# Kernel tuning notes

Measured on AMD Instinct MI355X. Metric: run time of the kernel, lower is better.

## Reference

```python
import jax, jax.numpy as jnp
import numpy as np
from jax import lax

B, T, C, H, W = 32, 64, 3, 32, 32
N_OBJS = 2
HID = 200
FEAT = N_OBJS * C * H * W  # 6*32*32 = 6144, matches LocationNetwork input


def setup_inputs() -> dict:
    key = jax.random.key(0)
    ks = jax.random.split(key, 20)

    def g(k, shape, scale):
        return jax.random.normal(k, shape, dtype=jnp.float32) * scale

    inp = {
        "x": jax.random.normal(ks[0], (B, C, H, W, T), dtype=jnp.float32),
        # shallow UNet (depth=3, base 8 channels): encoder
        "enc_w1": g(ks[1], (8, C, 3, 3), 0.2),  "enc_b1": jnp.zeros((8,), jnp.float32),
        "enc_w2": g(ks[2], (16, 8, 3, 3), 0.12), "enc_b2": jnp.zeros((16,), jnp.float32),
        "enc_w3": g(ks[3], (32, 16, 3, 3), 0.08),"enc_b3": jnp.zeros((32,), jnp.float32),
        # decoder (upsample + skip concat)
        "dec_w2": g(ks[4], (16, 48, 3, 3), 0.05), "dec_b2": jnp.zeros((16,), jnp.float32),
        "dec_w1": g(ks[5], (8, 24, 3, 3), 0.07),  "dec_b1": jnp.zeros((8,), jnp.float32),
        # final 1x1 conv -> n_objs mask logits
        "out_w": g(ks[6], (N_OBJS, 8, 1, 1), 0.3), "out_b": jnp.zeros((N_OBJS,), jnp.float32),
        # LocationNetwork: 6144 -> 200 -> 200 -> 2*n_objs
        "loc_w1": g(ks[7], (FEAT, HID), 0.013), "loc_b1": jnp.zeros((HID,), jnp.float32),
        "loc_w2": g(ks[8], (HID, HID), 0.07),   "loc_b2": jnp.zeros((HID,), jnp.float32),
        "loc_w3": g(ks[9], (HID, 2 * N_OBJS), 0.07), "loc_b3": jnp.zeros((2 * N_OBJS,), jnp.float32),
    }
    return inp


def _conv(h, w, b):
    return lax.conv_general_dilated(
        h, w, (1, 1), "SAME", dimension_numbers=("NCHW", "OIHW", "NCHW")
    ) + b[None, :, None, None]


def _pool(h):  # 2x2 max pool
    return lax.reduce_window(h, -jnp.inf, lax.max, (1, 1, 2, 2), (1, 1, 2, 2), "VALID")


def _up(h):
    return jnp.repeat(jnp.repeat(h, 2, axis=2), 2, axis=3)


def _forward(x, enc_w1, enc_b1, enc_w2, enc_b2, enc_w3, enc_b3,
             dec_w2, dec_b2, dec_w1, dec_b1, out_w, out_b,
             loc_w1, loc_b1, loc_w2, loc_b2, loc_w3, loc_b3):
    relu = jax.nn.relu
    # fold time into batch: [B,C,H,W,T] -> [B*T,C,H,W] (replaces per-t Python loop)
    xt = jnp.moveaxis(x, -1, 1).reshape(B * T, C, H, W)

    # shallow UNet, depth 3
    e1 = relu(_conv(xt, enc_w1, enc_b1))                 # [BT, 8, 32, 32]
    e2 = relu(_conv(_pool(e1), enc_w2, enc_b2))          # [BT,16, 16, 16]
    e3 = relu(_conv(_pool(e2), enc_w3, enc_b3))          # [BT,32,  8,  8]
    d2 = relu(_conv(jnp.concatenate([_up(e3), e2], 1), dec_w2, dec_b2))  # [BT,16,16,16]
    d1 = relu(_conv(jnp.concatenate([_up(d2), e1], 1), dec_w1, dec_b1))  # [BT, 8,32,32]
    logits = _conv(d1, out_w, out_b)                     # [BT, n_objs, 32, 32]

    # append ones channel, softmax over channels -> attention masks
    logits = jnp.concatenate([logits, jnp.ones_like(logits[:, :1])], axis=1)
    masks = jax.nn.softmax(logits, axis=1)               # [BT, n_objs+1, H, W]

    # masked_objs: mask_i * x, concatenated along channel dim
    masked = masks[:, :N_OBJS, None] * xt[:, None]       # [BT, n_objs, C, H, W]
    feat = masked.reshape(B * T, FEAT)                   # flatten per frame (6144)

    # LocationNetwork (batched over all B*T frames, replaces nested Python loops)
    h = jax.nn.relu(feat @ loc_w1 + loc_b1)
    h = jax.nn.relu(h @ loc_w2 + loc_b2)
    loc = h @ loc_w3 + loc_b3                            # [BT, 2*n_objs]

    loc = loc.reshape(B, T, N_OBJS, 2)
    # torch.split(h, n_objs, dim=1) + cat(dim=1) is an identity; squeeze(2) drops the
    # singleton from the per-frame reshape(-1, n_objs, 2)
    return jnp.tanh(loc) * (H / 2) + H / 2               # [B, T, n_objs, 2]


def reference(x, enc_w1, enc_b1, enc_w2, enc_b2, enc_w3, enc_b3,
              dec_w2, dec_b2, dec_w1, dec_b1, out_w, out_b,
              loc_w1, loc_b1, loc_w2, loc_b2, loc_w3, loc_b3):
    return _forward(x, enc_w1, enc_b1, enc_w2, enc_b2, enc_w3, enc_b3,
                    dec_w2, dec_b2, dec_w1, dec_b1, out_w, out_b,
                    loc_w1, loc_b1, loc_w2, loc_b2, loc_w3, loc_b3)
```

## Files before the change

kernel.cpp:

```cpp
#include <hip/hip_runtime.h>

constexpr int Bc = 32, Tc = 64, Cc = 3, Hc = 32, Wc = 32;
constexpr int F = Bc * Tc;
constexpr int FEATN = 2 * Cc * Hc * Wc;
constexpr int HID = 200;
constexpr int NP = 224;
constexpr int KSPLIT = 16;

typedef __attribute__((ext_vector_type(8))) short bf16x8;
typedef __attribute__((ext_vector_type(4))) float f32x4;

static __device__ __forceinline__ ushort f2bf(float x) {
    union { float f; unsigned u; } v; v.f = x;
    unsigned r = (v.u + 0x7FFF + ((v.u >> 16) & 1)) >> 16;
    return (ushort)r;
}

__global__ __launch_bounds__(256)
void transpose_kernel(const float* __restrict__ x, float* __restrict__ xt) {
    __shared__ float lds[32 * 65];
    int bid = blockIdx.x;
    int h = bid & 31;
    int c = (bid >> 5) % 3;
    int b = bid / (3 * 32);
    const float* src = x + (size_t)bid * 2048;
#pragma unroll
    for (int j = 0; j < 8; ++j) {
        int i = threadIdx.x + j * 256;
        lds[(i >> 6) * 65 + (i & 63)] = src[i];
    }
    __syncthreads();
#pragma unroll
    for (int j = 0; j < 8; ++j) {
        int i = threadIdx.x + j * 256;
        int t = i >> 5, w = i & 31;
        int f = b * 64 + t;
        xt[((size_t)(f * 3 + c) << 10) + h * 32 + w] = lds[w * 65 + t];
    }
}

template<int CIN1, int CIN2, int COUT, int H, int W, bool UP1, bool RELU>
__global__ __launch_bounds__(256)
void conv3x3_allco_kernel(const float* __restrict__ in1, const float* __restrict__ in2,
                          const float* __restrict__ wgt, const float* __restrict__ bias,
                          float* __restrict__ out) {
    constexpr int CTOT = CIN1 + CIN2;
    constexpr int NW = CTOT * 9 * COUT;
    constexpr int NCOG = COUT / 8;
    static_assert(COUT % 8 == 0, "COUT % 8");
    __shared__ __align__(16) float wl[NW];
    for (int i = threadIdx.x; i < NW; i += 256) {
        int co = i % COUT, r = i / COUT;
        wl[i] = wgt[co * CTOT * 9 + r];
    }
    __syncthreads();

    int tid = blockIdx.x * 256 + threadIdx.x;
    int x0  = tid % W;
    int y0  = (tid / W) % H;
    int cog = (tid / (W * H)) % NCOG;
    int f   = tid / (W * H * NCOG);

    float acc[8];
#pragma unroll
    for (int c = 0; c < 8; ++c) acc[c] = bias[cog * 8 + c];

    const float4* wl4 = reinterpret_cast<const float4*>(wl);
    const int wsel = cog * 2;

    for (int ci = 0; ci < CIN1; ++ci) {
        const float* ib;
        if (UP1) ib = in1 + (size_t)(f * CIN1 + ci) * (H / 2) * (W / 2);
        else     ib = in1 + (size_t)(f * CIN1 + ci) * H * W;
#pragma unroll
        for (int kh = 0; kh < 3; ++kh) {
            int yy = y0 + kh - 1;
            if (yy < 0 || yy >= H) continue;
#pragma unroll
            for (int kw = 0; kw < 3; ++kw) {
                int xx = x0 + kw - 1;
                if (xx < 0 || xx >= W) continue;
                float v;
                if (UP1) v = ib[(yy >> 1) * (W / 2) + (xx >> 1)];
                else     v = ib[yy * W + xx];
                int r = ci * 9 + kh * 3 + kw;
                float4 w0 = wl4[r * (COUT / 4) + wsel];
                float4 w1 = wl4[r * (COUT / 4) + wsel + 1];
                acc[0] = fmaf(v, w0.x, acc[0]); acc[1] = fmaf(v, w0.y, acc[1]);
                acc[2] = fmaf(v, w0.z, acc[2]); acc[3] = fmaf(v, w0.w, acc[3]);
                acc[4] = fmaf(v, w1.x, acc[4]); acc[5] = fmaf(v, w1.y, acc[5]);
                acc[6] = fmaf(v, w1.z, acc[6]); acc[7] = fmaf(v, w1.w, acc[7]);
            }
        }
    }
    if constexpr (CIN2 > 0) {
        for (int ci2 = 0; ci2 < CIN2; ++ci2) {
            const float* ib = in2 + (size_t)(f * CIN2 + ci2) * H * W;
#pragma unroll
            for (int kh = 0; kh < 3; ++kh) {
                int yy = y0 + kh - 1;
                if (yy < 0 || yy >= H) continue;
#pragma unroll
                for (int kw = 0; kw < 3; ++kw) {
                    int xx = x0 + kw - 1;
                    if (xx < 0 || xx >= W) continue;
                    float v = ib[yy * W + xx];
                    int r = (CIN1 + ci2) * 9 + kh * 3 + kw;
                    float4 w0 = wl4[r * (COUT / 4) + wsel];
                    float4 w1 = wl4[r * (COUT / 4) + wsel + 1];
                    acc[0] = fmaf(v, w0.x, acc[0]); acc[1] = fmaf(v, w0.y, acc[1]);
                    acc[2] = fmaf(v, w0.z, acc[2]); acc[3] = fmaf(v, w0.w, acc[3]);
                    acc[4] = fmaf(v, w1.x, acc[4]); acc[5] = fmaf(v, w1.y, acc[5]);
                    acc[6] = fmaf(v, w1.z, acc[6]); acc[7] = fmaf(v, w1.w, acc[7]);
                }
            }
        }
    }

    size_t ob = (size_t)(f * COUT + cog * 8) * (H * W) + y0 * W + x0;
#pragma unroll
    for (int c = 0; c < 8; ++c) {
        float vv = acc[c];
        if (RELU) vv = fmaxf(vv, 0.0f);
        out[ob + (size_t)c * (H * W)] = vv;
    }
}

template<int CIN1, int CIN2, int COUT, int H, int W, bool RELU>
__global__ __launch_bounds__(256)
void conv3x3_up_q22_kernel(const float* __restrict__ in1, const float* __restrict__ in2,
                           const float* __restrict__ wgt, const float* __restrict__ bias,
                           float* __restrict__ out) {
    constexpr int CTOT = CIN1 + CIN2;
    constexpr int NW = CTOT * 9 * COUT;
    constexpr int NCOG = COUT / 8;
    constexpr int H2 = H / 2, W2 = W / 2;
    static_assert(COUT % 8 == 0, "COUT % 8");
    __shared__ __align__(16) float wl[NW];
    for (int i = threadIdx.x; i < NW; i += 256) {
        int co = i % COUT, r = i / COUT;
        wl[i] = wgt[co * CTOT * 9 + r];
    }
    __syncthreads();

    int tid = blockIdx.x * 256 + threadIdx.x;
    int xq  = tid % W2;
    int yq  = (tid / W2) % H2;
    int cog = (tid / (W2 * H2)) % NCOG;
    int f   = tid / (W2 * H2 * NCOG);

    float acc[4][8];
#pragma unroll
    for (int p = 0; p < 4; ++p)
#pragma unroll
        for (int c = 0; c < 8; ++c) acc[p][c] = bias[cog * 8 + c];

    const float4* wl4 = reinterpret_cast<const float4*>(wl);
    const int wsel = cog * 2;

    const bool by0 = (yq > 0), by2 = (yq < H2 - 1);
    const bool bx0 = (xq > 0), bx2 = (xq < W2 - 1);
    const int ym = by0 ? yq - 1 : 0, yp = by2 ? yq + 1 : H2 - 1;
    const int xm = bx0 ? xq - 1 : 0, xp = bx2 ? xq + 1 : W2 - 1;

    for (int ci = 0; ci < CIN1; ++ci) {
        const float* ib = in1 + (size_t)(f * CIN1 + ci) * (H2 * W2);
        float s[3][3];
        s[0][0] = ib[ym * W2 + xm]; s[0][1] = ib[ym * W2 + xq]; s[0][2] = ib[ym * W2 + xp];
        s[1][0] = ib[yq * W2 + xm]; s[1][1] = ib[yq * W2 + xq]; s[1][2] = ib[yq * W2 + xp];
        s[2][0] = ib[yp * W2 + xm]; s[2][1] = ib[yp * W2 + xq]; s[2][2] = ib[yp * W2 + xp];
        s[0][0] = (by0 && bx0) ? s[0][0] : 0.f;
        s[0][1] = by0 ? s[0][1] : 0.f;
        s[0][2] = (by0 && bx2) ? s[0][2] : 0.f;
        s[1][0] = bx0 ? s[1][0] : 0.f;
        s[1][2] = bx2 ? s[1][2] : 0.f;
        s[2][0] = (by2 && bx0) ? s[2][0] : 0.f;
        s[2][1] = by2 ? s[2][1] : 0.f;
        s[2][2] = (by2 && bx2) ? s[2][2] : 0.f;
#pragma unroll
        for (int kh = 0; kh < 3; ++kh) {
#pragma unroll
            for (int kw = 0; kw < 3; ++kw) {
                int r = ci * 9 + kh * 3 + kw;
                float4 w0 = wl4[r * (COUT / 4) + wsel];
                float4 w1 = wl4[r * (COUT / 4) + wsel + 1];
#pragma unroll
                for (int dy = 0; dy < 2; ++dy) {
                    const int sy = (dy == 0) ? ((kh == 0) ? 0 : 1) : ((kh == 2) ? 2 : 1);
#pragma unroll
                    for (int dx = 0; dx < 2; ++dx) {
                        const int sx = (dx == 0) ? ((kw == 0) ? 0 : 1) : ((kw == 2) ? 2 : 1);
                        const float v = s[sy][sx];
                        float* a = acc[dy * 2 + dx];
                        a[0] = fmaf(v, w0.x, a[0]); a[1] = fmaf(v, w0.y, a[1]);
                        a[2] = fmaf(v, w0.z, a[2]); a[3] = fmaf(v, w0.w, a[3]);
                        a[4] = fmaf(v, w1.x, a[4]); a[5] = fmaf(v, w1.y, a[5]);
                        a[6] = fmaf(v, w1.z, a[6]); a[7] = fmaf(v, w1.w, a[7]);
                    }
                }
            }
        }
    }

    if constexpr (CIN2 > 0) {
        const int y2 = 2 * yq, x2 = 2 * xq;
        const int R0 = by0 ? y2 - 1 : 0, R3 = by2 ? y2 + 2 : H - 1;
        const int C0 = bx0 ? x2 - 1 : 0, C3 = bx2 ? x2 + 2 : W - 1;
        const int rr[4] = {R0, y2, y2 + 1, R3};
        const int cc[4] = {C0, x2, x2 + 1, C3};
        for (int ci2 = 0; ci2 < CIN2; ++ci2) {
            const float* ib = in2 + (size_t)(f * CIN2 + ci2) * (H * W);
            float t[4][4];
#pragma unroll
            for (int i = 0; i < 4; ++i)
#pragma unroll
                for (int j = 0; j < 4; ++j) t[i][j] = ib[rr[i] * W + cc[j]];
#pragma unroll
            for (int j = 0; j < 4; ++j) { t[0][j] = by0 ? t[0][j] : 0.f; t[3][j] = by2 ? t[3][j] : 0.f; }
#pragma unroll
            for (int i = 0; i < 4; ++i) { t[i][0] = bx0 ? t[i][0] : 0.f; t[i][3] = bx2 ? t[i][3] : 0.f; }
#pragma unroll
            for (int kh = 0; kh < 3; ++kh) {
#pragma unroll
                for (int kw = 0; kw < 3; ++kw) {
                    int r = (CIN1 + ci2) * 9 + kh * 3 + kw;
                    float4 w0 = wl4[r * (COUT / 4) + wsel];
                    float4 w1 = wl4[r * (COUT / 4) + wsel + 1];
#pragma unroll
                    for (int dy = 0; dy < 2; ++dy) {
#pragma unroll
                        for (int dx = 0; dx < 2; ++dx) {
                            const float v = t[dy + kh][dx + kw];
                            float* a = acc[dy * 2 + dx];
                            a[0] = fmaf(v, w0.x, a[0]); a[1] = fmaf(v, w0.y, a[1]);
                            a[2] = fmaf(v, w0.z, a[2]); a[3] = fmaf(v, w0.w, a[3]);
                            a[4] = fmaf(v, w1.x, a[4]); a[5] = fmaf(v, w1.y, a[5]);
                            a[6] = fmaf(v, w1.z, a[6]); a[7] = fmaf(v, w1.w, a[7]);
                        }
                    }
                }
            }
        }
    }

    const size_t ob = (size_t)(f * COUT + cog * 8) * (H * W);
#pragma unroll
    for (int dy = 0; dy < 2; ++dy)
#pragma unroll
        for (int dx = 0; dx < 2; ++dx) {
            const int p = dy * 2 + dx;
            const size_t pb = ob + (size_t)(2 * yq + dy) * W + (2 * xq + dx);
#pragma unroll
            for (int c = 0; c < 8; ++c) {
                float vv = acc[p][c];
                if (RELU) vv = fmaxf(vv, 0.0f);
                out[pb + (size_t)c * (H * W)] = vv;
            }
        }
}

template<int CH, int H, int W>
__global__ __launch_bounds__(256)
void pool2_kernel(const float* __restrict__ in, float* __restrict__ out) {
    int tid = blockIdx.x * 256 + threadIdx.x;
    constexpr int total = F * CH * (H / 2) * (W / 2);
    if (tid >= total) return;
    int x = tid % (W / 2);
    int y = (tid / (W / 2)) % (H / 2);
    int fc = tid / ((W / 2) * (H / 2));
    const float* ib = in + (size_t)fc * H * W + (2 * y) * W + 2 * x;
    float m = fmaxf(fmaxf(ib[0], ib[1]), fmaxf(ib[W], ib[W + 1]));
    out[tid] = m;
}

__global__ __launch_bounds__(256)
void maskfeat_kernel(const float* __restrict__ d1, const float* __restrict__ xt,
                     const float* __restrict__ ow, const float* __restrict__ ob,
                     ushort* __restrict__ feat) {
    int tid = blockIdx.x * 256 + threadIdx.x;
    if (tid >= F * 1024) return;
    int hw = tid & 1023;
    int f  = tid >> 10;
    const float* db = d1 + ((size_t)f << 13) + hw;
    float l0 = ob[0], l1 = ob[1];
#pragma unroll
    for (int c = 0; c < 8; ++c) {
        float v = db[c << 10];
        l0 = fmaf(v, ow[c], l0);
        l1 = fmaf(v, ow[8 + c], l1);
    }
    float mx = fmaxf(fmaxf(l0, l1), 1.0f);
    float e0 = expf(l0 - mx), e1 = expf(l1 - mx), e2 = expf(1.0f - mx);
    float inv = 1.0f / (e0 + e1 + e2);
    float m0 = e0 * inv, m1 = e1 * inv;
    const float* xb = xt + (size_t)f * 3072 + hw;
    ushort* fb = feat + (size_t)f * 6144 + hw;
#pragma unroll
    for (int c = 0; c < 3; ++c) {
        float xv = xb[c << 10];
        fb[c << 10]          = f2bf(m0 * xv);
        fb[3072 + (c << 10)] = f2bf(m1 * xv);
    }
}

__global__ __launch_bounds__(256)
void w1prep_kernel(const float* __restrict__ W, ushort* __restrict__ BT) {
    __shared__ float t[32][33];
    int kb = blockIdx.x % 192, nb = blockIdx.x / 192;
    int k0 = kb * 32, n0 = nb * 32;
    int r = threadIdx.x / 32, c = threadIdx.x % 32;
#pragma unroll
    for (int p = 0; p < 4; ++p) {
        int kk = r + p * 8;
        int n = n0 + c;
        t[kk][c] = (n < 200) ? W[(size_t)(k0 + kk) * 200 + n] : 0.0f;
    }
    __syncthreads();
#pragma unroll
    for (int p = 0; p < 4; ++p) {
        int nn = r + p * 8;
        BT[(size_t)(n0 + nn) * 6144 + k0 + c] = f2bf(t[c][nn]);
    }
}

__global__ __launch_bounds__(128)
void fc1_mfma_kernel(const ushort* __restrict__ A, const ushort* __restrict__ BT,
                     float* __restrict__ P) {
    int bid = blockIdx.x;
    int mb = bid & 15;
    int nb = (bid >> 4) % 7;
    int kc = bid / (16 * 7);
    int w = threadIdx.x >> 6, lane = threadIdx.x & 63;
    int m0 = mb * 128 + w * 64;
    int n0 = nb * 32;
    int row16 = lane & 15, kgrp = lane >> 4;

    f32x4 acc00 = {0,0,0,0}, acc01 = {0,0,0,0}, acc10 = {0,0,0,0}, acc11 = {0,0,0,0};
    f32x4 acc20 = {0,0,0,0}, acc21 = {0,0,0,0}, acc30 = {0,0,0,0}, acc31 = {0,0,0,0};

    const ushort* aB = A  + (size_t)(m0 + row16) * 6144 + kgrp * 8;
    const ushort* bB = BT + (size_t)(n0 + row16) * 6144 + kgrp * 8;
    int kend = kc * 384 + 384;
    for (int k = kc * 384; k < kend; k += 32) {
        bf16x8 b0 = *(const bf16x8*)(bB + k);
        bf16x8 b1 = *(const bf16x8*)(bB + 16 * 6144 + k);
        bf16x8 a0 = *(const bf16x8*)(aB + k);
        bf16x8 a1 = *(const bf16x8*)(aB + 16 * 6144 + k);
        bf16x8 a2 = *(const bf16x8*)(aB + 32 * 6144 + k);
        bf16x8 a3 = *(const bf16x8*)(aB + 48 * 6144 + k);
        acc00 = __builtin_amdgcn_mfma_f32_16x16x32_bf16(a0, b0, acc00, 0, 0, 0);
        acc01 = __builtin_amdgcn_mfma_f32_16x16x32_bf16(a0, b1, acc01, 0, 0, 0);
        acc10 = __builtin_amdgcn_mfma_f32_16x16x32_bf16(a1, b0, acc10, 0, 0, 0);
        acc11 = __builtin_amdgcn_mfma_f32_16x16x32_bf16(a1, b1, acc11, 0, 0, 0);
        acc20 = __builtin_amdgcn_mfma_f32_16x16x32_bf16(a2, b0, acc20, 0, 0, 0);
        acc21 = __builtin_amdgcn_mfma_f32_16x16x32_bf16(a2, b1, acc21, 0, 0, 0);
        acc30 = __builtin_amdgcn_mfma_f32_16x16x32_bf16(a3, b0, acc30, 0, 0, 0);
        acc31 = __builtin_amdgcn_mfma_f32_16x16x32_bf16(a3, b1, acc31, 0, 0, 0);
    }

    float* Pb = P + (size_t)kc * 2048 * NP;
    const f32x4* accs[4][2] = {{&acc00,&acc01},{&acc10,&acc11},{&acc20,&acc21},{&acc30,&acc31}};
#pragma unroll
    for (int s = 0; s < 4; ++s) {
#pragma unroll
        for (int h = 0; h < 2; ++h) {
            const f32x4 v = *accs[s][h];
#pragma unroll
            for (int r = 0; r < 4; ++r) {
                int m = m0 + s * 16 + kgrp * 4 + r;
                int n = n0 + h * 16 + row16;
                Pb[(size_t)m * NP + n] = v[r];
            }
        }
    }
}

__global__ __launch_bounds__(256)
void fc1_reduce_kernel(const float* __restrict__ P, const float* __restrict__ bias,
                       float* __restrict__ H1) {
    int tid = blockIdx.x * 256 + threadIdx.x;
    if (tid >= F * 200) return;
    int n = tid % 200, m = tid / 200;
    float s = bias[n];
#pragma unroll
    for (int kc = 0; kc < KSPLIT; ++kc)
        s += P[((size_t)kc * 2048 + m) * NP + n];
    H1[(size_t)m * 200 + n] = fmaxf(s, 0.0f);
}

template<int K, int BK>
__global__ __launch_bounds__(256)
void fc_tiled_kernel(const float* __restrict__ A, const float* __restrict__ Wm,
                     const float* __restrict__ bias, float* __restrict__ out) {
    constexpr int BM = 8, N = 200;
    static_assert(K % BK == 0, "K % BK");
    __shared__ float As[BM * BK];
    int t = threadIdx.x;
    int row0 = blockIdx.x * BM;
    int tx = t % 25, ty = t / 25;
    bool active = (ty < BM);
    int c0 = tx * 8;
    float acc0 = 0.f, acc1 = 0.f, acc2 = 0.f, acc3 = 0.f;
    float acc4 = 0.f, acc5 = 0.f, acc6 = 0.f, acc7 = 0.f;

    for (int kb = 0; kb < K; kb += BK) {
        for (int i = t; i < BM * BK; i += 256) {
            int r = i / BK, kk = i % BK;
            As[i] = A[(size_t)(row0 + r) * K + kb + kk];
        }
        __syncthreads();
        if (active) {
#pragma unroll
            for (int kk = 0; kk < BK; ++kk) {
                float a = As[ty * BK + kk];
                const float4* wp =
                    reinterpret_cast<const float4*>(Wm + (size_t)(kb + kk) * N + c0);
                float4 w0 = wp[0], w1 = wp[1];
                acc0 = fmaf(a, w0.x, acc0); acc1 = fmaf(a, w0.y, acc1);
                acc2 = fmaf(a, w0.z, acc2); acc3 = fmaf(a, w0.w, acc3);
                acc4 = fmaf(a, w1.x, acc4); acc5 = fmaf(a, w1.y, acc5);
                acc6 = fmaf(a, w1.z, acc6); acc7 = fmaf(a, w1.w, acc7);
            }
        }
        __syncthreads();
    }
    if (active) {
        const float4* bp = reinterpret_cast<const float4*>(bias + c0);
        float4 b0 = bp[0], b1 = bp[1];
        float4 o0, o1;
        o0.x = fmaxf(acc0 + b0.x, 0.f); o0.y = fmaxf(acc1 + b0.y, 0.f);
        o0.z = fmaxf(acc2 + b0.z, 0.f); o0.w = fmaxf(acc3 + b0.w, 0.f);
        o1.x = fmaxf(acc4 + b1.x, 0.f); o1.y = fmaxf(acc5 + b1.y, 0.f);
        o1.z = fmaxf(acc6 + b1.z, 0.f); o1.w = fmaxf(acc7 + b1.w, 0.f);
        float4* op = reinterpret_cast<float4*>(out + (size_t)(row0 + ty) * N + c0);
        op[0] = o0; op[1] = o1;
    }
}

__global__ __launch_bounds__(256)
void fc3_tanh_kernel(const float* __restrict__ A, const float* __restrict__ Wm,
                     const float* __restrict__ bias, float* __restrict__ out) {
    __shared__ float wl[800];
    int t = threadIdx.x;
#pragma unroll
    for (int j = 0; j < 4; ++j) {
        int i = t + j * 256;
        if (i < 800) wl[i] = Wm[i];
    }
    __syncthreads();
    int row = blockIdx.x * 256 + t;
    float a0 = bias[0], a1 = bias[1], a2 = bias[2], a3 = bias[3];
    const float* ar = A + (size_t)row * 200;
#pragma unroll 8
    for (int k = 0; k < 200; ++k) {
        float a = ar[k];
        const float4 w = *reinterpret_cast<const float4*>(&wl[k * 4]);
        a0 = fmaf(a, w.x, a0); a1 = fmaf(a, w.y, a1);
        a2 = fmaf(a, w.z, a2); a3 = fmaf(a, w.w, a3);
    }
    float4 o;
    o.x = tanhf(a0) * 16.0f + 16.0f;
    o.y = tanhf(a1) * 16.0f + 16.0f;
    o.z = tanhf(a2) * 16.0f + 16.0f;
    o.w = tanhf(a3) * 16.0f + 16.0f;
    *reinterpret_cast<float4*>(out + (size_t)row * 4) = o;
}

extern "C" void kernel_launch(void* const* d_in, const int* in_sizes, int n_in,
                              void* d_out, int out_size, void* d_ws, size_t ws_size,
                              hipStream_t stream) {
    const float* x      = (const float*)d_in[0];
    const float* enc_w1 = (const float*)d_in[1];
    const float* enc_b1 = (const float*)d_in[2];
    const float* enc_w2 = (const float*)d_in[3];
    const float* enc_b2 = (const float*)d_in[4];
    const float* enc_w3 = (const float*)d_in[5];
    const float* enc_b3 = (const float*)d_in[6];
    const float* dec_w2 = (const float*)d_in[7];
    const float* dec_b2 = (const float*)d_in[8];
    const float* dec_w1 = (const float*)d_in[9];
    const float* dec_b1 = (const float*)d_in[10];
    const float* out_w  = (const float*)d_in[11];
    const float* out_b  = (const float*)d_in[12];
    const float* loc_w1 = (const float*)d_in[13];
    const float* loc_b1 = (const float*)d_in[14];
    const float* loc_w2 = (const float*)d_in[15];
    const float* loc_b2 = (const float*)d_in[16];
    const float* loc_w3 = (const float*)d_in[17];
    const float* loc_b3 = (const float*)d_in[18];
    float* out = (float*)d_out;

    float* ws = (float*)d_ws;
    float* XT = ws;
    float* E1 = XT + 6291456;
    float* S  = E1 + 16777216;
    float* P  = S;
    float* E2 = S + 4194304;
    float* E3 = S + 4194304 + 8388608;
    float* D2 = S + 16777216;
    float* D1 = S;
    ushort* FEATB = (ushort*)E1;
    float* H1 = S;
    float* H2 = S + 409600;
    float* P16 = S + 819200;
    ushort* BT = (ushort*)(S + 8159232);
    (void)ws_size; (void)in_sizes; (void)n_in; (void)out_size;

    transpose_kernel<<<Bc * Cc * Hc, 256, 0, stream>>>(x, XT);

    conv3x3_allco_kernel<3, 0, 8, 32, 32, false, true><<<8192, 256, 0, stream>>>(
        XT, nullptr, enc_w1, enc_b1, E1);
    pool2_kernel<8, 32, 32><<<4194304 / 256, 256, 0, stream>>>(E1, P);
    conv3x3_allco_kernel<8, 0, 16, 16, 16, false, true><<<4096, 256, 0, stream>>>(
        P, nullptr, enc_w2, enc_b2, E2);
    pool2_kernel<16, 16, 16><<<2097152 / 256, 256, 0, stream>>>(E2, P);
    conv3x3_allco_kernel<16, 0, 32, 8, 8, false, true><<<2048, 256, 0, stream>>>(
        P, nullptr, enc_w3, enc_b3, E3);

    conv3x3_up_q22_kernel<32, 16, 16, 16, 16, true><<<1024, 256, 0, stream>>>(
        E3, E2, dec_w2, dec_b2, D2);
    conv3x3_up_q22_kernel<16, 8, 8, 32, 32, true><<<2048, 256, 0, stream>>>(
        D2, E1, dec_w1, dec_b1, D1);

    maskfeat_kernel<<<2097152 / 256, 256, 0, stream>>>(D1, XT, out_w, out_b, FEATB);

    w1prep_kernel<<<192 * 7, 256, 0, stream>>>(loc_w1, BT);
    fc1_mfma_kernel<<<16 * 7 * KSPLIT, 128, 0, stream>>>(FEATB, BT, P16);
    fc1_reduce_kernel<<<(F * 200 + 255) / 256, 256, 0, stream>>>(P16, loc_b1, H1);
    fc_tiled_kernel<HID, 40><<<F / 8, 256, 0, stream>>>(H1, loc_w2, loc_b2, H2);
    fc3_tanh_kernel<<<F / 256, 256, 0, stream>>>(H2, loc_w3, loc_b3, out);
}
```

Measured before the change: 617.9 us.

## Fuse maxpool into 2x2-quad encoder convs and simplify fc2 kernel

Encoder convolutions now compute a 2x2 output quad per thread from a shared 4x4 input tile, cutting redundant input loads and boundary branches. The 2x2 max pool is fused into the first two encoder convs' epilogues, removing two separate pool kernels and their global reads of E1/E2. The smem-tiled fc2 GEMM is replaced by a one-output-per-thread kernel that reads weights directly from global memory. The fc2 change may cost more global traffic, and the quad tiling raises register pressure.

```diff
diff --git a/kernel.cpp b/kernel.cpp
--- a/kernel.cpp
+++ b/kernel.cpp
@@ -39,90 +39,92 @@
     }
 }
 
-template<int CIN1, int CIN2, int COUT, int H, int W, bool UP1, bool RELU>
-__global__ __launch_bounds__(256)
-void conv3x3_allco_kernel(const float* __restrict__ in1, const float* __restrict__ in2,
-                          const float* __restrict__ wgt, const float* __restrict__ bias,
-                          float* __restrict__ out) {
-    constexpr int CTOT = CIN1 + CIN2;
-    constexpr int NW = CTOT * 9 * COUT;
+template<int CIN, int COUT, int H, int W, bool POOL>
+__global__ __launch_bounds__(256)
+void conv3x3_q22_kernel(const float* __restrict__ in,
+                        const float* __restrict__ wgt, const float* __restrict__ bias,
+                        float* __restrict__ out, float* __restrict__ pout) {
+    constexpr int NW = CIN * 9 * COUT;
     constexpr int NCOG = COUT / 8;
+    constexpr int H2 = H / 2, W2 = W / 2;
     static_assert(COUT % 8 == 0, "COUT % 8");
     __shared__ __align__(16) float wl[NW];
     for (int i = threadIdx.x; i < NW; i += 256) {
         int co = i % COUT, r = i / COUT;
-        wl[i] = wgt[co * CTOT * 9 + r];
+        wl[i] = wgt[co * CIN * 9 + r];
     }
     __syncthreads();
 
     int tid = blockIdx.x * 256 + threadIdx.x;
-    int x0  = tid % W;
-    int y0  = (tid / W) % H;
-    int cog = (tid / (W * H)) % NCOG;
-    int f   = tid / (W * H * NCOG);
-
-    float acc[8];
-#pragma unroll
-    for (int c = 0; c < 8; ++c) acc[c] = bias[cog * 8 + c];
+    int xq  = tid % W2;
+    int yq  = (tid / W2) % H2;
+    int cog = (tid / (W2 * H2)) % NCOG;
+    int f   = tid / (W2 * H2 * NCOG);
+
+    float acc[4][8];
+#pragma unroll
+    for (int p = 0; p < 4; ++p)
+#pragma unroll
+        for (int c = 0; c < 8; ++c) acc[p][c] = bias[cog * 8 + c];
 
     const float4* wl4 = reinterpret_cast<const float4*>(wl);
     const int wsel = cog * 2;
 
-    for (int ci = 0; ci < CIN1; ++ci) {
-        const float* ib;
-        if (UP1) ib = in1 + (size_t)(f * CIN1 + ci) * (H / 2) * (W / 2);
-        else     ib = in1 + (size_t)(f * CIN1 + ci) * H * W;
+    const bool by0 = (yq > 0), by2 = (yq < H2 - 1);
+    const bool bx0 = (xq > 0), bx2 = (xq < W2 - 1);
+    const int y2 = 2 * yq, x2 = 2 * xq;
+    const int R0 = by0 ? y2 - 1 : 0, R3 = by2 ? y2 + 2 : H - 1;
+    const int C0 = bx0 ? x2 - 1 : 0, C3 = bx2 ? x2 + 2 : W - 1;
+    const int rr[4] = {R0, y2, y2 + 1, R3};
+    const int cc[4] = {C0, x2, x2 + 1, C3};
+
+    for (int ci = 0; ci < CIN; ++ci) {
+        const float* ib = in + (size_t)(f * CIN + ci) * (H * W);
+        float t[4][4];
+#pragma unroll
+        for (int i = 0; i < 4; ++i)
+#pragma unroll
+            for (int j = 0; j < 4; ++j) t[i][j] = ib[rr[i] * W + cc[j]];
+#pragma unroll
+        for (int j = 0; j < 4; ++j) { t[0][j] = by0 ? t[0][j] : 0.f; t[3][j] = by2 ? t[3][j] : 0.f; }
+#pragma unroll
+        for (int i = 0; i < 4; ++i) { t[i][0] = bx0 ? t[i][0] : 0.f; t[i][3] = bx2 ? t[i][3] : 0.f; }
 #pragma unroll
         for (int kh = 0; kh < 3; ++kh) {
-            int yy = y0 + kh - 1;
-            if (yy < 0 || yy >= H) continue;
 #pragma unroll
             for (int kw = 0; kw < 3; ++kw) {
-                int xx = x0 + kw - 1;
-                if (xx < 0 || xx >= W) continue;
-                float v;
-                if (UP1) v = ib[(yy >> 1) * (W / 2) + (xx >> 1)];
-                else     v = ib[yy * W + xx];
                 int r = ci * 9 + kh * 3 + kw;
                 float4 w0 = wl4[r * (COUT / 4) + wsel];
                 float4 w1 = wl4[r * (COUT / 4) + wsel + 1];
-                acc[0] = fmaf(v, w0.x, acc[0]); acc[1] = fmaf(v, w0.y, acc[1]);
-                acc[2] = fmaf(v, w0.z, acc[2]); acc[3] = fmaf(v, w0.w, acc[3]);
-                acc[4] = fmaf(v, w1.x, acc[4]); acc[5] = fmaf(v, w1.y, acc[5]);
-                acc[6] = fmaf(v, w1.z, acc[6]); acc[7] = fmaf(v, w1.w, acc[7]);
-            }
-        }
-    }
-    if constexpr (CIN2 > 0) {
-        for (int ci2 = 0; ci2 < CIN2; ++ci2) {
-            const float* ib = in2 + (size_t)(f * CIN2 + ci2) * H * W;
-#pragma unroll
-            for (int kh = 0; kh < 3; ++kh) {
-                int yy = y0 + kh - 1;
-                if (yy < 0 || yy >= H) continue;
-#pragma unroll
-                for (int kw = 0; kw < 3; ++kw) {
-                    int xx = x0 + kw - 1;
-                    if (xx < 0 || xx >= W) continue;
-                    float v = ib[yy * W + xx];
-                    int r = (CIN1 + ci2) * 9 + kh * 3 + kw;
-                    float4 w0 = wl4[r * (COUT / 4) + wsel];
-                    float4 w1 = wl4[r * (COUT / 4) + wsel + 1];
-                    acc[0] = fmaf(v, w0.x, acc[0]); acc[1] = fmaf(v, w0.y, acc[1]);
-                    acc[2] = fmaf(v, w0.z, acc[2]); acc[3] = fmaf(v, w0.w, acc[3]);
-                    acc[4] = fmaf(v, w1.x, acc[4]); acc[5] = fmaf(v, w1.y, acc[5]);
-                    acc[6] = fmaf(v, w1.z, acc[6]); acc[7] = fmaf(v, w1.w, acc[7]);
+#pragma unroll
+                for (int dy = 0; dy < 2; ++dy) {
+#pragma unroll
+                    for (int dx = 0; dx < 2; ++dx) {
+                        const float v = t[dy + kh][dx + kw];
+                        float* a = acc[dy * 2 + dx];
+                        a[0] = fmaf(v, w0.x, a[0]); a[1] = fmaf(v, w0.y, a[1]);
+                        a[2] = fmaf(v, w0.z, a[2]); a[3] = fmaf(v, w0.w, a[3]);
+                        a[4] = fmaf(v, w1.x, a[4]); a[5] = fmaf(v, w1.y, a[5]);
+                        a[6] = fmaf(v, w1.z, a[6]); a[7] = fmaf(v, w1.w, a[7]);
+                    }
                 }
             }
         }
     }
 
-    size_t ob = (size_t)(f * COUT + cog * 8) * (H * W) + y0 * W + x0;
+    const size_t ob = (size_t)(f * COUT + cog * 8) * (H * W);
 #pragma unroll
     for (int c = 0; c < 8; ++c) {
-        float vv = acc[c];
-        if (RELU) vv = fmaxf(vv, 0.0f);
-        out[ob + (size_t)c * (H * W)] = vv;
+        float v00 = fmaxf(acc[0][c], 0.0f), v01 = fmaxf(acc[1][c], 0.0f);
+        float v10 = fmaxf(acc[2][c], 0.0f), v11 = fmaxf(acc[3][c], 0.0f);
+        const size_t cb = ob + (size_t)c * (H * W);
+        out[cb + (size_t)y2 * W + x2]           = v00;
+        out[cb + (size_t)y2 * W + x2 + 1]       = v01;
+        out[cb + (size_t)(y2 + 1) * W + x2]     = v10;
+        out[cb + (size_t)(y2 + 1) * W + x2 + 1] = v11;
+        if (POOL)
+            pout[(size_t)(f * COUT + cog * 8 + c) * (H2 * W2) + yq * W2 + xq] =
+                fmaxf(fmaxf(v00, v01), fmaxf(v10, v11));
     }
 }
 
@@ -257,20 +259,6 @@
                 out[pb + (size_t)c * (H * W)] = vv;
             }
         }
-}
-
-template<int CH, int H, int W>
-__global__ __launch_bounds__(256)
-void pool2_kernel(const float* __restrict__ in, float* __restrict__ out) {
-    int tid = blockIdx.x * 256 + threadIdx.x;
-    constexpr int total = F * CH * (H / 2) * (W / 2);
-    if (tid >= total) return;
-    int x = tid % (W / 2);
-    int y = (tid / (W / 2)) % (H / 2);
-    int fc = tid / ((W / 2) * (H / 2));
-    const float* ib = in + (size_t)fc * H * W + (2 * y) * W + 2 * x;
-    float m = fmaxf(fmaxf(ib[0], ib[1]), fmaxf(ib[W], ib[W + 1]));
-    out[tid] = m;
 }
 
 __global__ __launch_bounds__(256)
@@ -388,53 +376,22 @@
     H1[(size_t)m * 200 + n] = fmaxf(s, 0.0f);
 }
 
-template<int K, int BK>
-__global__ __launch_bounds__(256)
-void fc_tiled_kernel(const float* __restrict__ A, const float* __restrict__ Wm,
-                     const float* __restrict__ bias, float* __restrict__ out) {
-    constexpr int BM = 8, N = 200;
-    static_assert(K % BK == 0, "K % BK");
-    __shared__ float As[BM * BK];
-    int t = threadIdx.x;
-    int row0 = blockIdx.x * BM;
-    int tx = t % 25, ty = t / 25;
-    bool active = (ty < BM);
-    int c0 = tx * 8;
-    float acc0 = 0.f, acc1 = 0.f, acc2 = 0.f, acc3 = 0.f;
-    float acc4 = 0.f, acc5 = 0.f, acc6 = 0.f, acc7 = 0.f;
-
-    for (int kb = 0; kb < K; kb += BK) {
-        for (int i = t; i < BM * BK; i += 256) {
-            int r = i / BK, kk = i % BK;
-            As[i] = A[(size_t)(row0 + r) * K + kb + kk];
-        }
-        __syncthreads();
-        if (active) {
-#pragma unroll
-            for (int kk = 0; kk < BK; ++kk) {
-                float a = As[ty * BK + kk];
-                const float4* wp =
-                    reinterpret_cast<const float4*>(Wm + (size_t)(kb + kk) * N + c0);
-                float4 w0 = wp[0], w1 = wp[1];
-                acc0 = fmaf(a, w0.x, acc0); acc1 = fmaf(a, w0.y, acc1);
-                acc2 = fmaf(a, w0.z, acc2); acc3 = fmaf(a, w0.w, acc3);
-                acc4 = fmaf(a, w1.x, acc4); acc5 = fmaf(a, w1.y, acc5);
-                acc6 = fmaf(a, w1.z, acc6); acc7 = fmaf(a, w1.w, acc7);
-            }
-        }
-        __syncthreads();
-    }
-    if (active) {
-        const float4* bp = reinterpret_cast<const float4*>(bias + c0);
-        float4 b0 = bp[0], b1 = bp[1];
-        float4 o0, o1;
-        o0.x = fmaxf(acc0 + b0.x, 0.f); o0.y = fmaxf(acc1 + b0.y, 0.f);
-        o0.z = fmaxf(acc2 + b0.z, 0.f); o0.w = fmaxf(acc3 + b0.w, 0.f);
-        o1.x = fmaxf(acc4 + b1.x, 0.f); o1.y = fmaxf(acc5 + b1.y, 0.f);
-        o1.z = fmaxf(acc6 + b1.z, 0.f); o1.w = fmaxf(acc7 + b1.w, 0.f);
-        float4* op = reinterpret_cast<float4*>(out + (size_t)(row0 + ty) * N + c0);
-        op[0] = o0; op[1] = o1;
-    }
+__global__ __launch_bounds__(256)
+void fc2_kernel(const float* __restrict__ A, const float* __restrict__ Wm,
+                const float* __restrict__ bias, float* __restrict__ out) {
+    int tid = blockIdx.x * 256 + threadIdx.x;
+    if (tid >= F * 200) return;
+    int col = tid % 200, row = tid / 200;
+    const float* ar = A + (size_t)row * 200;
+    float s0 = 0.f, s1 = 0.f, s2 = 0.f, s3 = 0.f;
+#pragma unroll 2
+    for (int k = 0; k < 200; k += 4) {
+        s0 = fmaf(ar[k],     Wm[(size_t)k * 200 + col],       s0);
+        s1 = fmaf(ar[k + 1], Wm[(size_t)(k + 1) * 200 + col], s1);
+        s2 = fmaf(ar[k + 2], Wm[(size_t)(k + 2) * 200 + col], s2);
+        s3 = fmaf(ar[k + 3], Wm[(size_t)(k + 3) * 200 + col], s3);
+    }
+    out[tid] = fmaxf((s0 + s1) + (s2 + s3) + bias[col], 0.0f);
 }
 
 __global__ __launch_bounds__(256)
@@ -494,10 +451,11 @@
     float* XT = ws;
     float* E1 = XT + 6291456;
     float* S  = E1 + 16777216;
-    float* P  = S;
+    float* P1 = S;
     float* E2 = S + 4194304;
     float* E3 = S + 4194304 + 8388608;
     float* D2 = S + 16777216;
+    float* P2 = D2;
     float* D1 = S;
     ushort* FEATB = (ushort*)E1;
     float* H1 = S;
@@ -508,14 +466,12 @@
 
     transpose_kernel<<<Bc * Cc * Hc, 256, 0, stream>>>(x, XT);
 
-    conv3x3_allco_kernel<3, 0, 8, 32, 32, false, true><<<8192, 256, 0, stream>>>(
-        XT, nullptr, enc_w1, enc_b1, E1);
-    pool2_kernel<8, 32, 32><<<4194304 / 256, 256, 0, stream>>>(E1, P);
-    conv3x3_allco_kernel<8, 0, 16, 16, 16, false, true><<<4096, 256, 0, stream>>>(
-        P, nullptr, enc_w2, enc_b2, E2);
-    pool2_kernel<16, 16, 16><<<2097152 / 256, 256, 0, stream>>>(E2, P);
-    conv3x3_allco_kernel<16, 0, 32, 8, 8, false, true><<<2048, 256, 0, stream>>>(
-        P, nullptr, enc_w3, enc_b3, E3);
+    conv3x3_q22_kernel<3, 8, 32, 32, true><<<2048, 256, 0, stream>>>(
+        XT, enc_w1, enc_b1, E1, P1);
+    conv3x3_q22_kernel<8, 16, 16, 16, true><<<1024, 256, 0, stream>>>(
+        P1, enc_w2, enc_b2, E2, P2);
+    conv3x3_q22_kernel<16, 32, 8, 8, false><<<512, 256, 0, stream>>>(
+        P2, enc_w3, enc_b3, E3, nullptr);
 
     conv3x3_up_q22_kernel<32, 16, 16, 16, 16, true><<<1024, 256, 0, stream>>>(
         E3, E2, dec_w2, dec_b2, D2);
@@ -527,6 +483,6 @@
     w1prep_kernel<<<192 * 7, 256, 0, stream>>>(loc_w1, BT);
     fc1_mfma_kernel<<<16 * 7 * KSPLIT, 128, 0, stream>>>(FEATB, BT, P16);
     fc1_reduce_kernel<<<(F * 200 + 255) / 256, 256, 0, stream>>>(P16, loc_b1, H1);
-    fc_tiled_kernel<HID, 40><<<F / 8, 256, 0, stream>>>(H1, loc_w2, loc_b2, H2);
+    fc2_kernel<<<(F * 200 + 255) / 256, 256, 0, stream>>>(H1, loc_w2, loc_b2, H2);
     fc3_tanh_kernel<<<F / 256, 256, 0, stream>>>(H2, loc_w3, loc_b3, out);
 }
```

Result: faster. 546.6 us (-11.6%).
